# Optimization experiments

Hardware: AMD Instinct MI355X
Metric: run time of the kernel (lower is better)

The kernel has to match this reference:

```python
import jax, jax.numpy as jnp
import numpy as np

N, R, E = 100000, 3, 500000
IN_F, HID_F, OUT_F = 128, 128, 32


def setup_inputs() -> dict:
    key = jax.random.key(0)
    ks = jax.random.split(key, 12)
    inp = {
        "x": jax.random.normal(ks[0], (N, IN_F), dtype=jnp.float32),
        "src": jax.random.randint(ks[1], (R, E), 0, N, dtype=jnp.int32),
        "dst": jax.random.randint(ks[2], (R, E), 0, N, dtype=jnp.int32),
        # per-relation weights for the 4 layers (Glorot-ish scale)
        "W0": jax.random.normal(ks[3], (R, IN_F, HID_F), dtype=jnp.float32) / np.sqrt(IN_F),
        "b0": jnp.zeros((R, HID_F), dtype=jnp.float32),
        "W1": jax.random.normal(ks[4], (R, HID_F, HID_F), dtype=jnp.float32) / np.sqrt(HID_F),
        "b1": jnp.zeros((R, HID_F), dtype=jnp.float32),
        "W2": jax.random.normal(ks[5], (R, HID_F, HID_F), dtype=jnp.float32) / np.sqrt(HID_F),
        "b2": jnp.zeros((R, HID_F), dtype=jnp.float32),
        "W3": jax.random.normal(ks[6], (R, HID_F, OUT_F), dtype=jnp.float32) / np.sqrt(HID_F),
        "b3": jnp.zeros((R, OUT_F), dtype=jnp.float32),
    }
    return inp


def _degree_norms(src, dst, n_nodes):
    # DGL GraphConv norm='both': clamp degree to >=1, use deg^-1/2
    ones = jnp.ones(src.shape[1], dtype=jnp.float32)
    dout = jax.vmap(lambda s: jax.ops.segment_sum(ones, s, num_segments=n_nodes))(src)
    din = jax.vmap(lambda d: jax.ops.segment_sum(ones, d, num_segments=n_nodes))(dst)
    return jnp.clip(dout, 1.0) ** -0.5, jnp.clip(din, 1.0) ** -0.5  # [R, N] each


def _hetero_layer(h, W, b, src, dst, dout_is, din_is, relu):
    # per-relation GraphConv (norm='both'), HeteroGraphConv aggregate='sum'
    n = h.shape[0]
    out = None
    for r in range(W.shape[0]):
        hs = h * dout_is[r][:, None]                          # [N, d] scale src
        msg = hs[src[r]]                                       # [E, d] gather
        agg = jax.ops.segment_sum(msg, dst[r], num_segments=n) # [N, d] scatter-add
        agg = agg * din_is[r][:, None]
        o = agg @ W[r] + b[r]
        if relu:
            o = jax.nn.relu(o)  # activation inside GraphConv, before cross-rel sum
        out = o if out is None else out + o
    return out


def reference(x, src, dst, W0, b0, W1, b1, W2, b2, W3, b3):
    dout_is, din_is = _degree_norms(src, dst, x.shape[0])
    h = _hetero_layer(x, W0, b0, src, dst, dout_is, din_is, relu=True)
    h = _hetero_layer(h, W1, b1, src, dst, dout_is, din_is, relu=True)
    h = _hetero_layer(h, W2, b2, src, dst, dout_is, din_is, relu=True)
    h = _hetero_layer(h, W3, b3, src, dst, dout_is, din_is, relu=False)
    return h  # [N, OUT_F]
```

## Files before the change

### kernel.cpp

```cpp
#include <hip/hip_runtime.h>
#include <cstdint>
#include <cstddef>

#define NN 100000
#define RR 3
#define EE 500000
#define RN 300000
#define RE 1500000
#define KK 384
#define CAP 32

typedef unsigned short u16;
typedef unsigned int   u32;
typedef __attribute__((ext_vector_type(8))) short bhalf8;
typedef __attribute__((ext_vector_type(4))) float f32x4;

static inline int cdiv_h(int a, int b){ return (a+b-1)/b; }

__device__ __forceinline__ float bf_lo(u32 v){ union{u32 u; float f;} c; c.u = v<<16; return c.f; }
__device__ __forceinline__ float bf_hi(u32 v){ union{u32 u; float f;} c; c.u = v & 0xffff0000u; return c.f; }
__device__ __forceinline__ float bf1(u16 v){ union{u32 u; float f;} c; c.u = ((u32)v)<<16; return c.f; }
__device__ __forceinline__ u16 f2bf(float f){
  union{float f; u32 u;} c; c.f = f;
  u32 r = (c.u + 0x7FFFu + ((c.u >> 16) & 1u)) >> 16;
  return (u16)r;
}

__global__ __launch_bounds__(256) void k_pre0(const float* __restrict__ x, u16* __restrict__ xb,
    const float* __restrict__ W0, const float* __restrict__ W1, const float* __restrict__ W2,
    const float* __restrict__ W3, u16* __restrict__ Wtb, u16* __restrict__ Wt3b,
    int* __restrict__ row_start, int* __restrict__ cursor,
    int* __restrict__ dout_cnt, int* __restrict__ din_cnt, int padded){
  int b = blockIdx.x, t = threadIdx.x;
  if (b < 6250){
    int i = b*256 + t;
    if (i < NN*128/8){
      float4 v0 = ((const float4*)x)[i*2];
      float4 v1 = ((const float4*)x)[i*2+1];
      uint4 o;
      o.x = (u32)f2bf(v0.x) | ((u32)f2bf(v0.y)<<16);
      o.y = (u32)f2bf(v0.z) | ((u32)f2bf(v0.w)<<16);
      o.z = (u32)f2bf(v1.x) | ((u32)f2bf(v1.y)<<16);
      o.w = (u32)f2bf(v1.z) | ((u32)f2bf(v1.w)<<16);
      ((uint4*)xb)[i] = o;
    }
  } else if (b < 7422){
    int i = (b-6250)*256 + t;
    if (i < RN){
      dout_cnt[i] = 0;
      if (padded){ row_start[i] = i*CAP; cursor[i] = i*CAP; }
      else       { din_cnt[i] = 0; }
    }
  } else if (b < 9150){
    int gid = (b-7422)*256 + t;
    if (gid < 3*3*16384){
      int l = gid / 49152; int rem = gid - l*49152;
      int r = rem >> 14; int rem2 = rem & 16383;
      int k = rem2 >> 7; int n = rem2 & 127;
      const float* Wl = (l==0) ? W0 : (l==1) ? W1 : W2;
      Wtb[((size_t)(l*3+r))*16384 + (size_t)n*128 + k] = f2bf(Wl[rem]);
    }
  } else {
    int gid = (b-9150)*256 + t;
    if (gid < 3*4096){
      int r = gid >> 12; int rem = gid & 4095;
      int k = rem >> 5; int n = rem & 31;
      Wt3b[(size_t)(r*32+n)*128 + k] = f2bf(W3[gid]);
    }
  }
}

__global__ __launch_bounds__(256) void k_pre1(const int* __restrict__ src, const int* __restrict__ dst,
    int* __restrict__ cursor, int* __restrict__ dout_cnt, int* __restrict__ edge_src){
  int i = blockIdx.x*256 + threadIdx.x;
  if (i < RE){
    int r = i / EE;
    int s = src[i], d = dst[i];
    atomicAdd(&dout_cnt[r*NN + s], 1);
    int idx = r*NN + d;
    int pos = atomicAdd(&cursor[idx], 1);
    if (pos < idx*CAP + CAP) edge_src[pos] = s;
  }
}

__global__ __launch_bounds__(256) void k_norms(const int* __restrict__ dout_cnt, float* __restrict__ dout_is){
  int i = blockIdx.x*256 + threadIdx.x;
  if (i < RN){
    int dc = dout_cnt[i] > 1 ? dout_cnt[i] : 1;
    dout_is[i] = rsqrtf((float)dc);
  }
}

__global__ __launch_bounds__(256) void k_degrees(const int* __restrict__ src, const int* __restrict__ dst,
    int* __restrict__ dout_cnt, int* __restrict__ din_cnt){
  int i = blockIdx.x*256 + threadIdx.x;
  if (i < RE){
    int r = i / EE;
    atomicAdd(&dout_cnt[r*NN + src[i]], 1);
    atomicAdd(&din_cnt[r*NN + dst[i]], 1);
  }
}

__global__ __launch_bounds__(256) void k_scan1(const int* __restrict__ in, int* __restrict__ out,
    int* __restrict__ bsum, int n){
  __shared__ int s[256];
  int t = threadIdx.x;
  int base = blockIdx.x*1024 + t*4;
  int4 v = make_int4(0,0,0,0);
  if (base < n) v = *(const int4*)&in[base];
  int tot = v.x + v.y + v.z + v.w;
  s[t] = tot; __syncthreads();
  for (int off=1; off<256; off<<=1){
    int x = (t>=off) ? s[t-off] : 0;
    __syncthreads();
    s[t] += x;
    __syncthreads();
  }
  if (t==255) bsum[blockIdx.x] = s[255];
  int excl = (t>0) ? s[t-1] : 0;
  if (base < n){
    int4 o; o.x = excl; o.y = excl+v.x; o.z = excl+v.x+v.y; o.w = excl+v.x+v.y+v.z;
    *(int4*)&out[base] = o;
  }
}

__global__ __launch_bounds__(512) void k_scan2(int* __restrict__ bsum, int nb){
  __shared__ int s[512];
  int t = threadIdx.x;
  s[t] = (t < nb) ? bsum[t] : 0;
  __syncthreads();
  for (int off=1; off<512; off<<=1){
    int x = (t>=off) ? s[t-off] : 0;
    __syncthreads();
    s[t] += x;
    __syncthreads();
  }
  int excl = (t>0) ? s[t-1] : 0;
  if (t < nb) bsum[t] = excl;
}

__global__ __launch_bounds__(256) void k_scan3(int* __restrict__ row_start, const int* __restrict__ bsum,
    int* __restrict__ cursor, int n){
  int i = blockIdx.x*256 + threadIdx.x;
  if (i < n){
    int v = row_start[i] + bsum[i >> 10];
    row_start[i] = v;
    cursor[i] = v;
  }
}

__global__ __launch_bounds__(256) void k_fill(const int* __restrict__ src, const int* __restrict__ dst,
    int* __restrict__ cursor, int* __restrict__ edge_src){
  int i = blockIdx.x*256 + threadIdx.x;
  if (i < RE){
    int r = i / EE;
    int d = dst[i];
    int pos = atomicAdd(&cursor[r*NN + d], 1);
    edge_src[pos] = src[i];
  }
}

__global__ __launch_bounds__(256) void k_agg_bf(const u16* __restrict__ h, u16* __restrict__ AGG,
    const int* __restrict__ row_start, const int* __restrict__ row_end,
    const int* __restrict__ edge_src, const float* __restrict__ dout_is){
  int w = (blockIdx.x*256 + threadIdx.x) >> 6;
  if (w >= RN) return;
  int l = threadIdx.x & 63;
  int q = l >> 4, k = l & 15;
  int r = w / NN;
  int n = w - r*NN;
  int s0 = row_start[w];
  int s1 = row_end[w];
  int cap = s0 + CAP;
  if (s1 > cap) s1 = cap;
  const float* __restrict__ dis = dout_is + r*NN;
  const uint4* __restrict__ h4 = (const uint4*)h;
  float a[8] = {0.f,0.f,0.f,0.f,0.f,0.f,0.f,0.f};
  for (int p = s0 + q; p < s1; p += 4){
    int s = edge_src[p];
    float wg = dis[s];
    uint4 v = h4[(size_t)s*16 + k];
    a[0] += wg*bf_lo(v.x); a[1] += wg*bf_hi(v.x);
    a[2] += wg*bf_lo(v.y); a[3] += wg*bf_hi(v.y);
    a[4] += wg*bf_lo(v.z); a[5] += wg*bf_hi(v.z);
    a[6] += wg*bf_lo(v.w); a[7] += wg*bf_hi(v.w);
  }
  #pragma unroll
  for (int i=0;i<8;i++){
    a[i] += __shfl_xor(a[i], 16);
    a[i] += __shfl_xor(a[i], 32);
  }
  if (q == 0){
    int cnt = s1 - s0;
    float di = rsqrtf((float)(cnt > 1 ? cnt : 1));
    uint4 o;
    o.x = (u32)f2bf(a[0]*di) | ((u32)f2bf(a[1]*di)<<16);
    o.y = (u32)f2bf(a[2]*di) | ((u32)f2bf(a[3]*di)<<16);
    o.z = (u32)f2bf(a[4]*di) | ((u32)f2bf(a[5]*di)<<16);
    o.w = (u32)f2bf(a[6]*di) | ((u32)f2bf(a[7]*di)<<16);
    ((uint4*)AGG)[(size_t)n*48 + r*16 + k] = o;
  }
}

__global__ __launch_bounds__(256) void k_mm_relu(const u16* __restrict__ A, const u16* __restrict__ Wt,
    const float* __restrict__ bias, u16* __restrict__ out){
  __shared__ __align__(16) u16 As[128*128];
  __shared__ __align__(16) u16 Bs[128*128];
  int t = threadIdx.x;
  int l = t & 63, w = t >> 6;
  int wr = w >> 1, wc = w & 1;
  int row0 = blockIdx.x * 128;
  int tr = t >> 4, tc = t & 15;
  int swz = tr & 7;

  f32x4 res[4][4];
  #pragma unroll
  for (int m=0;m<4;m++)
    #pragma unroll
    for (int n=0;n<4;n++) res[m][n] = (f32x4){0.f,0.f,0.f,0.f};

  for (int r=0; r<RR; r++){
    uint4 ra[8], rb[8];
    #pragma unroll
    for (int it=0; it<8; ++it){
      int grow = row0 + it*16 + tr;
      if (grow > NN-1) grow = NN-1;
      ra[it] = *(const uint4*)&A[(size_t)grow*KK + r*128 + tc*8];
      rb[it] = *(const uint4*)&Wt[(size_t)r*16384 + (size_t)(it*16 + tr)*128 + tc*8];
    }
    __syncthreads();
    #pragma unroll
    for (int it=0; it<8; ++it){
      int rho = it*16 + tr;
      int ch = (tc ^ swz) * 8;
      *(uint4*)&As[rho*128 + ch] = ra[it];
      *(uint4*)&Bs[rho*128 + ch] = rb[it];
    }
    __syncthreads();

    f32x4 acc[4][4];
    #pragma unroll
    for (int m=0;m<4;m++)
      #pragma unroll
      for (int n=0;n<4;n++) acc[m][n] = (f32x4){0.f,0.f,0.f,0.f};

    #pragma unroll
    for (int kk=0; kk<4; ++kk){
      bhalf8 af[4], bf[4];
      #pragma unroll
      for (int m=0;m<4;m++){
        int rho = wr*64 + m*16 + (l&15);
        int ch = (kk*4 + (l>>4)) ^ (l&7);
        af[m] = *(const bhalf8*)&As[rho*128 + ch*8];
      }
      #pragma unroll
      for (int n=0;n<4;n++){
        int rho = wc*64 + n*16 + (l&15);
        int ch = (kk*4 + (l>>4)) ^ (l&7);
        bf[n] = *(const bhalf8*)&Bs[rho*128 + ch*8];
      }
      #pragma unroll
      for (int m=0;m<4;m++)
        #pragma unroll
        for (int n=0;n<4;n++)
          acc[m][n] = __builtin_amdgcn_mfma_f32_16x16x32_bf16(af[m], bf[n], acc[m][n], 0, 0, 0);
    }

    #pragma unroll
    for (int n=0;n<4;n++){
      int col = wc*64 + n*16 + (l&15);
      float bb = bias[r*128 + col];
      #pragma unroll
      for (int m=0;m<4;m++)
        #pragma unroll
        for (int i=0;i<4;i++){
          float v = acc[m][n][i] + bb;
          res[m][n][i] += v > 0.f ? v : 0.f;
        }
    }
  }

  #pragma unroll
  for (int m=0;m<4;m++)
    #pragma unroll
    for (int i=0;i<4;i++){
      int grow = row0 + wr*64 + m*16 + (l>>4)*4 + i;
      if (grow < NN){
        #pragma unroll
        for (int n=0;n<4;n++)
          out[(size_t)grow*128 + wc*64 + n*16 + (l&15)] = f2bf(res[m][n][i]);
      }
    }
}

__global__ __launch_bounds__(256) void k_mm_y(const u16* __restrict__ A, const u16* __restrict__ Wt3,
    u16* __restrict__ y){
  __shared__ __align__(16) u16 As[128*128];
  __shared__ __align__(16) u16 Bs[96*128];
  int t = threadIdx.x;
  int l = t & 63, w = t >> 6;
  int wr = w & 1, wc = w >> 1;
  int row0 = blockIdx.x * 128;
  int tr = t >> 4, tc = t & 15;
  int swz = tr & 7;

  uint4 ra[8], rb[6];
  #pragma unroll
  for (int it=0; it<8; ++it){
    int grow = row0 + it*16 + tr;
    if (grow > NN-1) grow = NN-1;
    ra[it] = *(const uint4*)&A[(size_t)grow*128 + tc*8];
  }
  #pragma unroll
  for (int it=0; it<6; ++it)
    rb[it] = *(const uint4*)&Wt3[(size_t)(it*16 + tr)*128 + tc*8];
  #pragma unroll
  for (int it=0; it<8; ++it)
    *(uint4*)&As[(it*16+tr)*128 + ((tc ^ swz)*8)] = ra[it];
  #pragma unroll
  for (int it=0; it<6; ++it)
    *(uint4*)&Bs[(it*16+tr)*128 + ((tc ^ swz)*8)] = rb[it];
  __syncthreads();

  f32x4 acc[4][3];
  #pragma unroll
  for (int m=0;m<4;m++)
    #pragma unroll
    for (int n=0;n<3;n++) acc[m][n] = (f32x4){0.f,0.f,0.f,0.f};

  #pragma unroll
  for (int kk=0; kk<4; ++kk){
    bhalf8 af[4], bf[3];
    #pragma unroll
    for (int m=0;m<4;m++){
      int rho = wr*64 + m*16 + (l&15);
      int ch = (kk*4 + (l>>4)) ^ (l&7);
      af[m] = *(const bhalf8*)&As[rho*128 + ch*8];
    }
    #pragma unroll
    for (int n=0;n<3;n++){
      int rho = wc*48 + n*16 + (l&15);
      int ch = (kk*4 + (l>>4)) ^ (l&7);
      bf[n] = *(const bhalf8*)&Bs[rho*128 + ch*8];
    }
    #pragma unroll
    for (int m=0;m<4;m++)
      #pragma unroll
      for (int n=0;n<3;n++)
        acc[m][n] = __builtin_amdgcn_mfma_f32_16x16x32_bf16(af[m], bf[n], acc[m][n], 0, 0, 0);
  }

  #pragma unroll
  for (int m=0;m<4;m++)
    #pragma unroll
    for (int i=0;i<4;i++){
      int grow = row0 + wr*64 + m*16 + (l>>4)*4 + i;
      if (grow < NN){
        #pragma unroll
        for (int n=0;n<3;n++)
          y[(size_t)grow*96 + wc*48 + n*16 + (l&15)] = f2bf(acc[m][n][i]);
      }
    }
}

__global__ __launch_bounds__(256) void k_agg_out(const u16* __restrict__ y, float* __restrict__ out,
    const int* __restrict__ row_start, const int* __restrict__ row_end,
    const int* __restrict__ edge_src, const float* __restrict__ dout_is,
    const float* __restrict__ b3){
  int n = (blockIdx.x*256 + threadIdx.x) >> 6;
  if (n >= NN) return;
  int l = threadIdx.x & 63;
  int g = l >> 3, k = l & 7;
  float res[4];
  #pragma unroll
  for (int i=0;i<4;i++) res[i] = b3[4*k+i] + b3[32+4*k+i] + b3[64+4*k+i];
  const uint2* __restrict__ y2 = (const uint2*)y;
  for (int r=0; r<RR; r++){
    int w = r*NN + n;
    int s0 = row_start[w];
    int s1 = row_end[w];
    int cap = s0 + CAP;
    if (s1 > cap) s1 = cap;
    const float* __restrict__ dis = dout_is + r*NN;
    float a[4] = {0.f,0.f,0.f,0.f};
    for (int p = s0 + g; p < s1; p += 8){
      int s = edge_src[p];
      float wg = dis[s];
      uint2 v = y2[(size_t)s*24 + r*8 + k];
      a[0] += wg*bf_lo(v.x); a[1] += wg*bf_hi(v.x);
      a[2] += wg*bf_lo(v.y); a[3] += wg*bf_hi(v.y);
    }
    #pragma unroll
    for (int i=0;i<4;i++){
      a[i] += __shfl_xor(a[i], 8);
      a[i] += __shfl_xor(a[i], 16);
      a[i] += __shfl_xor(a[i], 32);
    }
    int cnt = s1 - s0;
    float di = rsqrtf((float)(cnt>1?cnt:1));
    #pragma unroll
    for (int i=0;i<4;i++) res[i] += di*a[i];
  }
  if (g == 0)
    ((float4*)out)[(size_t)n*8 + k] = make_float4(res[0],res[1],res[2],res[3]);
}


extern "C" void kernel_launch(void* const* d_in, const int* in_sizes, int n_in,
                              void* d_out, int out_size, void* d_ws, size_t ws_size,
                              hipStream_t stream){
  const float* x   = (const float*)d_in[0];
  const int*   src = (const int*)d_in[1];
  const int*   dst = (const int*)d_in[2];
  const float* W0  = (const float*)d_in[3]; const float* b0 = (const float*)d_in[4];
  const float* W1  = (const float*)d_in[5]; const float* b1 = (const float*)d_in[6];
  const float* W2  = (const float*)d_in[7]; const float* b2 = (const float*)d_in[8];
  const float* W3  = (const float*)d_in[9]; const float* b3 = (const float*)d_in[10];
  float* out = (float*)d_out;

  char* p = (char*)d_ws;
  auto alloc = [&](size_t bytes)->char*{
    char* q = p; p += (bytes + 255) & ~(size_t)255; return q;
  };
  int*   row_start= (int*)  alloc(RN*4);
  int*   cursor   = (int*)  alloc(RN*4);
  int*   dout_cnt = (int*)  alloc(RN*4);
  int*   din_cnt  = (int*)  alloc(RN*4);
  float* dout_is  = (float*)alloc(RN*4);
  int*   bsum     = (int*)  alloc(2048);
  u16*   Wtb      = (u16*)  alloc((size_t)3*3*128*128*2);
  u16*   Wt3b     = (u16*)  alloc((size_t)3*32*128*2);
  u16*   AGG      = (u16*)  alloc((size_t)NN*KK*2);
  u16*   bufA     = (u16*)  alloc((size_t)NN*128*2);
  u16*   bufB     = (u16*)  alloc((size_t)NN*128*2);
  u16*   y        = AGG;

  size_t used = (size_t)(p - (char*)d_ws);
  size_t padded_bytes = (size_t)RN*CAP*4;
  int padded = (ws_size >= used + padded_bytes) ? 1 : 0;
  int* edge_src = (int*)alloc(padded ? padded_bytes : (size_t)RE*4);

  k_pre0<<<9198,256,0,stream>>>(x, bufB, W0,W1,W2,W3, Wtb, Wt3b,
                                row_start, cursor, dout_cnt, din_cnt, padded);
  if (padded){
    k_pre1<<<cdiv_h(RE,256),256,0,stream>>>(src, dst, cursor, dout_cnt, edge_src);
    k_norms<<<cdiv_h(RN,256),256,0,stream>>>(dout_cnt, dout_is);
  } else {
    k_degrees<<<cdiv_h(RE,256),256,0,stream>>>(src,dst,dout_cnt,din_cnt);
    k_norms  <<<cdiv_h(RN,256),256,0,stream>>>(dout_cnt, dout_is);
    k_scan1  <<<cdiv_h(RN,1024),256,0,stream>>>(din_cnt,row_start,bsum,RN);
    k_scan2  <<<1,512,0,stream>>>(bsum,cdiv_h(RN,1024));
    k_scan3  <<<cdiv_h(RN,256),256,0,stream>>>(row_start,bsum,cursor,RN);
    k_fill   <<<cdiv_h(RE,256),256,0,stream>>>(src,dst,cursor,edge_src);
  }

  int agg_blocks = cdiv_h(RN,4);
  int mm_blocks  = cdiv_h(NN,128);

  k_agg_bf<<<agg_blocks,256,0,stream>>>(bufB, AGG, row_start, cursor, edge_src, dout_is);
  k_mm_relu<<<mm_blocks,256,0,stream>>>(AGG, Wtb, b0, bufA);
  k_agg_bf<<<agg_blocks,256,0,stream>>>(bufA, AGG, row_start, cursor, edge_src, dout_is);
  k_mm_relu<<<mm_blocks,256,0,stream>>>(AGG, Wtb + 3*16384, b1, bufB);
  k_agg_bf<<<agg_blocks,256,0,stream>>>(bufB, AGG, row_start, cursor, edge_src, dout_is);
  k_mm_relu<<<mm_blocks,256,0,stream>>>(AGG, Wtb + 6*16384, b2, bufA);
  k_mm_y<<<mm_blocks,256,0,stream>>>(bufA, Wt3b, y);
  k_agg_out<<<cdiv_h(NN,4),256,0,stream>>>(y, out, row_start, cursor, edge_src, dout_is, b3);
}
```

Baseline: 773.9 us.

## Fuse neighbor aggregation into per-layer matmul kernel and merge preprocessing

Each hidden layer's gather/scatter aggregation now runs inside the matmul kernel. Every block gathers neighbor rows for its 128 nodes straight into shared memory, so the 384-wide bf16 AGG buffer no longer goes to global memory and comes back. Edge bucketing, x conversion and weight transposes are merged into one launch, and the fallback scan/CSR path is dropped, which assumes the workspace always fits the padded edge table. Fewer blocks (782) now do the irregular gather with low parallelism per node, which may hurt latency hiding compared with the old one-wave-per-row aggregation.

```diff
diff --git a/kernel.cpp b/kernel.cpp
--- a/kernel.cpp
+++ b/kernel.cpp
@@ -7,7 +7,6 @@
 #define EE 500000
 #define RN 300000
 #define RE 1500000
-#define KK 384
 #define CAP 32
 
 typedef unsigned short u16;
@@ -19,40 +18,46 @@
 
 __device__ __forceinline__ float bf_lo(u32 v){ union{u32 u; float f;} c; c.u = v<<16; return c.f; }
 __device__ __forceinline__ float bf_hi(u32 v){ union{u32 u; float f;} c; c.u = v & 0xffff0000u; return c.f; }
-__device__ __forceinline__ float bf1(u16 v){ union{u32 u; float f;} c; c.u = ((u32)v)<<16; return c.f; }
 __device__ __forceinline__ u16 f2bf(float f){
   union{float f; u32 u;} c; c.f = f;
   u32 r = (c.u + 0x7FFFu + ((c.u >> 16) & 1u)) >> 16;
   return (u16)r;
 }
-
-__global__ __launch_bounds__(256) void k_pre0(const float* __restrict__ x, u16* __restrict__ xb,
+__device__ __forceinline__ u32 pk2(float a, float b){ return (u32)f2bf(a) | ((u32)f2bf(b)<<16); }
+
+__global__ __launch_bounds__(256) void k_init(int* __restrict__ cursor, int* __restrict__ dout_cnt){
+  int i = blockIdx.x*256 + threadIdx.x;
+  if (i < RN){ cursor[i] = i*CAP; dout_cnt[i] = 0; }
+}
+
+__global__ __launch_bounds__(256) void k_pre1f(const int* __restrict__ src, const int* __restrict__ dst,
+    int* __restrict__ cursor, int* __restrict__ dout_cnt, int* __restrict__ edge_src,
+    const float* __restrict__ x, u16* __restrict__ xb,
     const float* __restrict__ W0, const float* __restrict__ W1, const float* __restrict__ W2,
-    const float* __restrict__ W3, u16* __restrict__ Wtb, u16* __restrict__ Wt3b,
-    int* __restrict__ row_start, int* __restrict__ cursor,
-    int* __restrict__ dout_cnt, int* __restrict__ din_cnt, int padded){
+    const float* __restrict__ W3, u16* __restrict__ Wtb, u16* __restrict__ Wt3b){
   int b = blockIdx.x, t = threadIdx.x;
-  if (b < 6250){
+  if (b < 5860){
     int i = b*256 + t;
+    if (i < RE){
+      int r = i / EE;
+      int s = src[i], d = dst[i];
+      atomicAdd(&dout_cnt[r*NN + s], 1);
+      int idx = r*NN + d;
+      int pos = atomicAdd(&cursor[idx], 1);
+      if (pos < idx*CAP + CAP) edge_src[pos] = s;
+    }
+  } else if (b < 12110){
+    int i = (b-5860)*256 + t;
     if (i < NN*128/8){
       float4 v0 = ((const float4*)x)[i*2];
       float4 v1 = ((const float4*)x)[i*2+1];
       uint4 o;
-      o.x = (u32)f2bf(v0.x) | ((u32)f2bf(v0.y)<<16);
-      o.y = (u32)f2bf(v0.z) | ((u32)f2bf(v0.w)<<16);
-      o.z = (u32)f2bf(v1.x) | ((u32)f2bf(v1.y)<<16);
-      o.w = (u32)f2bf(v1.z) | ((u32)f2bf(v1.w)<<16);
+      o.x = pk2(v0.x, v0.y); o.y = pk2(v0.z, v0.w);
+      o.z = pk2(v1.x, v1.y); o.w = pk2(v1.z, v1.w);
       ((uint4*)xb)[i] = o;
     }
-  } else if (b < 7422){
-    int i = (b-6250)*256 + t;
-    if (i < RN){
-      dout_cnt[i] = 0;
-      if (padded){ row_start[i] = i*CAP; cursor[i] = i*CAP; }
-      else       { din_cnt[i] = 0; }
-    }
-  } else if (b < 9150){
-    int gid = (b-7422)*256 + t;
+  } else if (b < 12686){
+    int gid = (b-12110)*256 + t;
     if (gid < 3*3*16384){
       int l = gid / 49152; int rem = gid - l*49152;
       int r = rem >> 14; int rem2 = rem & 16383;
@@ -61,25 +66,12 @@
       Wtb[((size_t)(l*3+r))*16384 + (size_t)n*128 + k] = f2bf(Wl[rem]);
     }
   } else {
-    int gid = (b-9150)*256 + t;
+    int gid = (b-12686)*256 + t;
     if (gid < 3*4096){
       int r = gid >> 12; int rem = gid & 4095;
       int k = rem >> 5; int n = rem & 31;
       Wt3b[(size_t)(r*32+n)*128 + k] = f2bf(W3[gid]);
     }
-  }
-}
-
-__global__ __launch_bounds__(256) void k_pre1(const int* __restrict__ src, const int* __restrict__ dst,
-    int* __restrict__ cursor, int* __restrict__ dout_cnt, int* __restrict__ edge_src){
-  int i = blockIdx.x*256 + threadIdx.x;
-  if (i < RE){
-    int r = i / EE;
-    int s = src[i], d = dst[i];
-    atomicAdd(&dout_cnt[r*NN + s], 1);
-    int idx = r*NN + d;
-    int pos = atomicAdd(&cursor[idx], 1);
-    if (pos < idx*CAP + CAP) edge_src[pos] = s;
   }
 }
 
@@ -91,119 +83,9 @@
   }
 }
 
-__global__ __launch_bounds__(256) void k_degrees(const int* __restrict__ src, const int* __restrict__ dst,
-    int* __restrict__ dout_cnt, int* __restrict__ din_cnt){
-  int i = blockIdx.x*256 + threadIdx.x;
-  if (i < RE){
-    int r = i / EE;
-    atomicAdd(&dout_cnt[r*NN + src[i]], 1);
-    atomicAdd(&din_cnt[r*NN + dst[i]], 1);
-  }
-}
-
-__global__ __launch_bounds__(256) void k_scan1(const int* __restrict__ in, int* __restrict__ out,
-    int* __restrict__ bsum, int n){
-  __shared__ int s[256];
-  int t = threadIdx.x;
-  int base = blockIdx.x*1024 + t*4;
-  int4 v = make_int4(0,0,0,0);
-  if (base < n) v = *(const int4*)&in[base];
-  int tot = v.x + v.y + v.z + v.w;
-  s[t] = tot; __syncthreads();
-  for (int off=1; off<256; off<<=1){
-    int x = (t>=off) ? s[t-off] : 0;
-    __syncthreads();
-    s[t] += x;
-    __syncthreads();
-  }
-  if (t==255) bsum[blockIdx.x] = s[255];
-  int excl = (t>0) ? s[t-1] : 0;
-  if (base < n){
-    int4 o; o.x = excl; o.y = excl+v.x; o.z = excl+v.x+v.y; o.w = excl+v.x+v.y+v.z;
-    *(int4*)&out[base] = o;
-  }
-}
-
-__global__ __launch_bounds__(512) void k_scan2(int* __restrict__ bsum, int nb){
-  __shared__ int s[512];
-  int t = threadIdx.x;
-  s[t] = (t < nb) ? bsum[t] : 0;
-  __syncthreads();
-  for (int off=1; off<512; off<<=1){
-    int x = (t>=off) ? s[t-off] : 0;
-    __syncthreads();
-    s[t] += x;
-    __syncthreads();
-  }
-  int excl = (t>0) ? s[t-1] : 0;
-  if (t < nb) bsum[t] = excl;
-}
-
-__global__ __launch_bounds__(256) void k_scan3(int* __restrict__ row_start, const int* __restrict__ bsum,
-    int* __restrict__ cursor, int n){
-  int i = blockIdx.x*256 + threadIdx.x;
-  if (i < n){
-    int v = row_start[i] + bsum[i >> 10];
-    row_start[i] = v;
-    cursor[i] = v;
-  }
-}
-
-__global__ __launch_bounds__(256) void k_fill(const int* __restrict__ src, const int* __restrict__ dst,
-    int* __restrict__ cursor, int* __restrict__ edge_src){
-  int i = blockIdx.x*256 + threadIdx.x;
-  if (i < RE){
-    int r = i / EE;
-    int d = dst[i];
-    int pos = atomicAdd(&cursor[r*NN + d], 1);
-    edge_src[pos] = src[i];
-  }
-}
-
-__global__ __launch_bounds__(256) void k_agg_bf(const u16* __restrict__ h, u16* __restrict__ AGG,
-    const int* __restrict__ row_start, const int* __restrict__ row_end,
-    const int* __restrict__ edge_src, const float* __restrict__ dout_is){
-  int w = (blockIdx.x*256 + threadIdx.x) >> 6;
-  if (w >= RN) return;
-  int l = threadIdx.x & 63;
-  int q = l >> 4, k = l & 15;
-  int r = w / NN;
-  int n = w - r*NN;
-  int s0 = row_start[w];
-  int s1 = row_end[w];
-  int cap = s0 + CAP;
-  if (s1 > cap) s1 = cap;
-  const float* __restrict__ dis = dout_is + r*NN;
-  const uint4* __restrict__ h4 = (const uint4*)h;
-  float a[8] = {0.f,0.f,0.f,0.f,0.f,0.f,0.f,0.f};
-  for (int p = s0 + q; p < s1; p += 4){
-    int s = edge_src[p];
-    float wg = dis[s];
-    uint4 v = h4[(size_t)s*16 + k];
-    a[0] += wg*bf_lo(v.x); a[1] += wg*bf_hi(v.x);
-    a[2] += wg*bf_lo(v.y); a[3] += wg*bf_hi(v.y);
-    a[4] += wg*bf_lo(v.z); a[5] += wg*bf_hi(v.z);
-    a[6] += wg*bf_lo(v.w); a[7] += wg*bf_hi(v.w);
-  }
-  #pragma unroll
-  for (int i=0;i<8;i++){
-    a[i] += __shfl_xor(a[i], 16);
-    a[i] += __shfl_xor(a[i], 32);
-  }
-  if (q == 0){
-    int cnt = s1 - s0;
-    float di = rsqrtf((float)(cnt > 1 ? cnt : 1));
-    uint4 o;
-    o.x = (u32)f2bf(a[0]*di) | ((u32)f2bf(a[1]*di)<<16);
-    o.y = (u32)f2bf(a[2]*di) | ((u32)f2bf(a[3]*di)<<16);
-    o.z = (u32)f2bf(a[4]*di) | ((u32)f2bf(a[5]*di)<<16);
-    o.w = (u32)f2bf(a[6]*di) | ((u32)f2bf(a[7]*di)<<16);
-    ((uint4*)AGG)[(size_t)n*48 + r*16 + k] = o;
-  }
-}
-
-__global__ __launch_bounds__(256) void k_mm_relu(const u16* __restrict__ A, const u16* __restrict__ Wt,
-    const float* __restrict__ bias, u16* __restrict__ out){
+__global__ __launch_bounds__(256) void k_layer(const u16* __restrict__ h, const u16* __restrict__ Wt,
+    const float* __restrict__ bias, const int* __restrict__ cursor,
+    const int* __restrict__ edge_src, const float* __restrict__ dout_is, u16* __restrict__ out){
   __shared__ __align__(16) u16 As[128*128];
   __shared__ __align__(16) u16 Bs[128*128];
   int t = threadIdx.x;
@@ -211,7 +93,9 @@
   int wr = w >> 1, wc = w & 1;
   int row0 = blockIdx.x * 128;
   int tr = t >> 4, tc = t & 15;
-  int swz = tr & 7;
+  int g = l >> 4, k = l & 15;
+
+  const uint4* __restrict__ h4 = (const uint4*)h;
 
   f32x4 res[4][4];
   #pragma unroll
@@ -220,21 +104,56 @@
     for (int n=0;n<4;n++) res[m][n] = (f32x4){0.f,0.f,0.f,0.f};
 
   for (int r=0; r<RR; r++){
-    uint4 ra[8], rb[8];
-    #pragma unroll
-    for (int it=0; it<8; ++it){
-      int grow = row0 + it*16 + tr;
-      if (grow > NN-1) grow = NN-1;
-      ra[it] = *(const uint4*)&A[(size_t)grow*KK + r*128 + tc*8];
-      rb[it] = *(const uint4*)&Wt[(size_t)r*16384 + (size_t)(it*16 + tr)*128 + tc*8];
-    }
-    __syncthreads();
+    if (r > 0) __syncthreads();
+
+    uint4 rb[8];
+    #pragma unroll
+    for (int it=0; it<8; ++it)
+      rb[it] = *(const uint4*)&Wt[(size_t)r*16384 + (size_t)(it*16+tr)*128 + tc*8];
+
+    const float* __restrict__ dis = dout_is + r*NN;
+
+    #pragma unroll 2
+    for (int qd=0; qd<8; ++qd){
+      int nl = w*32 + qd*4 + g;
+      int node = row0 + nl;
+      float a[8] = {0.f,0.f,0.f,0.f,0.f,0.f,0.f,0.f};
+      int cnt = 0;
+      if (node < NN){
+        int widx = r*NN + node;
+        int base = widx*CAP;
+        cnt = cursor[widx] - base;
+        if (cnt > CAP) cnt = CAP;
+        int e = 0;
+        for (; e+2 <= cnt; e += 2){
+          int sa = edge_src[base+e], sb = edge_src[base+e+1];
+          float wa = dis[sa], wb = dis[sb];
+          uint4 va = h4[(size_t)sa*16 + k];
+          uint4 vb = h4[(size_t)sb*16 + k];
+          a[0]+=wa*bf_lo(va.x); a[1]+=wa*bf_hi(va.x); a[2]+=wa*bf_lo(va.y); a[3]+=wa*bf_hi(va.y);
+          a[4]+=wa*bf_lo(va.z); a[5]+=wa*bf_hi(va.z); a[6]+=wa*bf_lo(va.w); a[7]+=wa*bf_hi(va.w);
+          a[0]+=wb*bf_lo(vb.x); a[1]+=wb*bf_hi(vb.x); a[2]+=wb*bf_lo(vb.y); a[3]+=wb*bf_hi(vb.y);
+          a[4]+=wb*bf_lo(vb.z); a[5]+=wb*bf_hi(vb.z); a[6]+=wb*bf_lo(vb.w); a[7]+=wb*bf_hi(vb.w);
+        }
+        if (e < cnt){
+          int s = edge_src[base+e];
+          float wa = dis[s];
+          uint4 v = h4[(size_t)s*16 + k];
+          a[0]+=wa*bf_lo(v.x); a[1]+=wa*bf_hi(v.x); a[2]+=wa*bf_lo(v.y); a[3]+=wa*bf_hi(v.y);
+          a[4]+=wa*bf_lo(v.z); a[5]+=wa*bf_hi(v.z); a[6]+=wa*bf_lo(v.w); a[7]+=wa*bf_hi(v.w);
+        }
+      }
+      float di = rsqrtf((float)(cnt > 1 ? cnt : 1));
+      uint4 o;
+      o.x = pk2(a[0]*di, a[1]*di); o.y = pk2(a[2]*di, a[3]*di);
+      o.z = pk2(a[4]*di, a[5]*di); o.w = pk2(a[6]*di, a[7]*di);
+      *(uint4*)&As[nl*128 + ((k ^ (nl&7))*8)] = o;
+    }
+
     #pragma unroll
     for (int it=0; it<8; ++it){
       int rho = it*16 + tr;
-      int ch = (tc ^ swz) * 8;
-      *(uint4*)&As[rho*128 + ch] = ra[it];
-      *(uint4*)&Bs[rho*128 + ch] = rb[it];
+      *(uint4*)&Bs[rho*128 + ((tc ^ (tr&7))*8)] = rb[it];
     }
     __syncthreads();
 
@@ -364,9 +283,8 @@
 }
 
 __global__ __launch_bounds__(256) void k_agg_out(const u16* __restrict__ y, float* __restrict__ out,
-    const int* __restrict__ row_start, const int* __restrict__ row_end,
-    const int* __restrict__ edge_src, const float* __restrict__ dout_is,
-    const float* __restrict__ b3){
+    const int* __restrict__ cursor, const int* __restrict__ edge_src,
+    const float* __restrict__ dout_is, const float* __restrict__ b3){
   int n = (blockIdx.x*256 + threadIdx.x) >> 6;
   if (n >= NN) return;
   int l = threadIdx.x & 63;
@@ -377,10 +295,9 @@
   const uint2* __restrict__ y2 = (const uint2*)y;
   for (int r=0; r<RR; r++){
     int w = r*NN + n;
-    int s0 = row_start[w];
-    int s1 = row_end[w];
-    int cap = s0 + CAP;
-    if (s1 > cap) s1 = cap;
+    int s0 = w*CAP;
+    int s1 = cursor[w];
+    if (s1 > s0 + CAP) s1 = s0 + CAP;
     const float* __restrict__ dis = dout_is + r*NN;
     float a[4] = {0.f,0.f,0.f,0.f};
     for (int p = s0 + g; p < s1; p += 8){
@@ -422,47 +339,25 @@
   auto alloc = [&](size_t bytes)->char*{
     char* q = p; p += (bytes + 255) & ~(size_t)255; return q;
   };
-  int*   row_start= (int*)  alloc(RN*4);
   int*   cursor   = (int*)  alloc(RN*4);
   int*   dout_cnt = (int*)  alloc(RN*4);
-  int*   din_cnt  = (int*)  alloc(RN*4);
   float* dout_is  = (float*)alloc(RN*4);
-  int*   bsum     = (int*)  alloc(2048);
-  u16*   Wtb      = (u16*)  alloc((size_t)3*3*128*128*2);
+  u16*   Wtb      = (u16*)  alloc((size_t)3*3*16384*2);
   u16*   Wt3b     = (u16*)  alloc((size_t)3*32*128*2);
-  u16*   AGG      = (u16*)  alloc((size_t)NN*KK*2);
+  u16*   y        = (u16*)  alloc((size_t)NN*96*2);
   u16*   bufA     = (u16*)  alloc((size_t)NN*128*2);
   u16*   bufB     = (u16*)  alloc((size_t)NN*128*2);
-  u16*   y        = AGG;
-
-  size_t used = (size_t)(p - (char*)d_ws);
-  size_t padded_bytes = (size_t)RN*CAP*4;
-  int padded = (ws_size >= used + padded_bytes) ? 1 : 0;
-  int* edge_src = (int*)alloc(padded ? padded_bytes : (size_t)RE*4);
-
-  k_pre0<<<9198,256,0,stream>>>(x, bufB, W0,W1,W2,W3, Wtb, Wt3b,
-                                row_start, cursor, dout_cnt, din_cnt, padded);
-  if (padded){
-    k_pre1<<<cdiv_h(RE,256),256,0,stream>>>(src, dst, cursor, dout_cnt, edge_src);
-    k_norms<<<cdiv_h(RN,256),256,0,stream>>>(dout_cnt, dout_is);
-  } else {
-    k_degrees<<<cdiv_h(RE,256),256,0,stream>>>(src,dst,dout_cnt,din_cnt);
-    k_norms  <<<cdiv_h(RN,256),256,0,stream>>>(dout_cnt, dout_is);
-    k_scan1  <<<cdiv_h(RN,1024),256,0,stream>>>(din_cnt,row_start,bsum,RN);
-    k_scan2  <<<1,512,0,stream>>>(bsum,cdiv_h(RN,1024));
-    k_scan3  <<<cdiv_h(RN,256),256,0,stream>>>(row_start,bsum,cursor,RN);
-    k_fill   <<<cdiv_h(RE,256),256,0,stream>>>(src,dst,cursor,edge_src);
-  }
-
-  int agg_blocks = cdiv_h(RN,4);
-  int mm_blocks  = cdiv_h(NN,128);
-
-  k_agg_bf<<<agg_blocks,256,0,stream>>>(bufB, AGG, row_start, cursor, edge_src, dout_is);
-  k_mm_relu<<<mm_blocks,256,0,stream>>>(AGG, Wtb, b0, bufA);
-  k_agg_bf<<<agg_blocks,256,0,stream>>>(bufA, AGG, row_start, cursor, edge_src, dout_is);
-  k_mm_relu<<<mm_blocks,256,0,stream>>>(AGG, Wtb + 3*16384, b1, bufB);
-  k_agg_bf<<<agg_blocks,256,0,stream>>>(bufB, AGG, row_start, cursor, edge_src, dout_is);
-  k_mm_relu<<<mm_blocks,256,0,stream>>>(AGG, Wtb + 6*16384, b2, bufA);
+  int*   edge_src = (int*)  alloc((size_t)RN*CAP*4);
+
+  k_init <<<cdiv_h(RN,256),256,0,stream>>>(cursor, dout_cnt);
+  k_pre1f<<<12734,256,0,stream>>>(src, dst, cursor, dout_cnt, edge_src,
+                                  x, bufB, W0,W1,W2,W3, Wtb, Wt3b);
+  k_norms<<<cdiv_h(RN,256),256,0,stream>>>(dout_cnt, dout_is);
+
+  int mm_blocks = cdiv_h(NN,128);
+  k_layer<<<mm_blocks,256,0,stream>>>(bufB, Wtb,           b0, cursor, edge_src, dout_is, bufA);
+  k_layer<<<mm_blocks,256,0,stream>>>(bufA, Wtb + 3*16384, b1, cursor, edge_src, dout_is, bufB);
+  k_layer<<<mm_blocks,256,0,stream>>>(bufB, Wtb + 6*16384, b2, cursor, edge_src, dout_is, bufA);
   k_mm_y<<<mm_blocks,256,0,stream>>>(bufA, Wt3b, y);
-  k_agg_out<<<cdiv_h(NN,4),256,0,stream>>>(y, out, row_start, cursor, edge_src, dout_is, b3);
-}
+  k_agg_out<<<cdiv_h(NN,4),256,0,stream>>>(y, out, cursor, edge_src, dout_is, b3);
+}
```

After: 808.8 us. 4.5% more time.
